# Kernel tuning notes

Hardware: AMD Instinct MI355X
Metric: run time of the kernel (lower is better)

Reference implementation:

```python
import jax, jax.numpy as jnp
import numpy as np

B, T, NE = 8, 4096, 1024
E, TOPK = 16, 2
LIN = NE + 32 + NE // 4 + NE // 4 + NE // 8 + NE // 8  # 1824
N_CITIES = 4


def setup_inputs() -> dict:
    key = jax.random.key(0)
    ks = jax.random.split(key, 11)
    s = 1.0 / np.sqrt(LIN)
    return {
        "mh_output": jax.random.normal(ks[0], (B, T, NE), jnp.float32),
        "delta_t_info": jax.random.normal(ks[1], (B, T, NE // 4), jnp.float32),
        "delta_dis_info": jax.random.normal(ks[2], (B, T, NE // 4), jnp.float32),
        "delta_rg_info": jax.random.normal(ks[3], (B, T, NE // 8), jnp.float32),
        "delta_entropy_info": jax.random.normal(ks[4], (B, T, NE // 8), jnp.float32),
        "city_embeddings": jax.random.normal(ks[5], (N_CITIES, 32), jnp.float32),
        "w_route": jax.random.uniform(ks[6], (LIN, E), jnp.float32, -s, s),
        "b_route": jax.random.uniform(ks[7], (E,), jnp.float32, -s, s),
        "w_noise": jax.random.uniform(ks[8], (LIN, E), jnp.float32, -s, s),
        "b_noise": jax.random.uniform(ks[9], (E,), jnp.float32, -s, s),
        "noise_eps": jax.random.normal(ks[10], (B, T, E), jnp.float32),
        "city_index": 0,
    }


def reference(mh_output, delta_t_info, delta_dis_info, delta_rg_info,
              delta_entropy_info, city_embeddings, w_route, b_route,
              w_noise, b_noise, noise_eps, city_index):
    b, t, _ = mh_output.shape
    city_embed = city_embeddings[city_index]  # [32]
    city_embeds = jnp.broadcast_to(city_embed[None, None, :], (b, t, 32))
    x = jnp.concatenate([mh_output, city_embeds, delta_t_info, delta_dis_info,
                         delta_rg_info, delta_entropy_info], axis=-1)  # [B,T,LIN]
    logits = jnp.einsum('btf,fe->bte', x, w_route) + b_route
    noise_logits = jnp.einsum('btf,fe->bte', x, w_noise) + b_noise
    noisy_logits = logits + noise_eps * jax.nn.softplus(noise_logits)  # training path
    gate1 = jax.nn.softmax(noisy_logits, axis=-1)
    top_k_logits, indices = jax.lax.top_k(noisy_logits, TOPK)  # [B,T,K]
    # scatter top-k values into a -inf tensor == mask non-topk entries to -inf
    mask = jnp.sum(jax.nn.one_hot(indices, noisy_logits.shape[-1], dtype=jnp.bool_), axis=-2) > 0
    sparse_logits = jnp.where(mask, noisy_logits, -jnp.inf)
    router_output = jax.nn.softmax(sparse_logits, axis=-1)
    return router_output, indices, gate1
```

## Files before the change

### kernel.cpp

```cpp
#include <hip/hip_runtime.h>
#include <math.h>


#define TOKS 128
#define NCHUNK 28
#define I_OFF 524288
#define G_OFF 589824
#define SA 68
#define SW 36
#define SS 36

__device__ __forceinline__ float softplus_f(float x) {
  return fmaxf(x, 0.0f) + log1pf(expf(-fabsf(x)));
}

__device__ __forceinline__ float get_comp(const float4& v, int kk) {
  return kk == 0 ? v.x : kk == 1 ? v.y : kk == 2 ? v.z : v.w;
}

__global__ __launch_bounds__(512, 2) void router_kernel(
    const float* __restrict__ mh, const float* __restrict__ dt,
    const float* __restrict__ dd, const float* __restrict__ rg,
    const float* __restrict__ de, const float* __restrict__ cemb_all,
    const float* __restrict__ w_route, const float* __restrict__ b_route,
    const float* __restrict__ w_noise, const float* __restrict__ b_noise,
    const float* __restrict__ eps, const int* __restrict__ city_index,
    float* __restrict__ out) {
  __shared__ float smem[22016];
  __shared__ float city_l[32];
  float* sA0 = smem;
  float* sA1 = smem + 8704;
  float* sW0 = smem + 17408;
  float* sW1 = smem + 19712;
  float* sS  = smem;

  const int tid = threadIdx.x;
  const int w   = tid >> 6;
  const int ln  = tid & 63;
  const int tg  = ln & 15;
  const int eg  = ln >> 4;
  const int blockTok = blockIdx.x * TOKS;

  if (tid < 32) {
    const int e = tid & 15;
    const float* wsrc = (tid < 16) ? w_route : w_noise;
    const float* bsrc = (tid < 16) ? b_route : b_noise;
    const float* ce = cemb_all + city_index[0] * 32;
    float s = bsrc[e];
#pragma unroll
    for (int j = 0; j < 32; ++j) s = fmaf(ce[j], wsrc[(1024 + j) * 16 + e], s);
    city_l[tid] = s;
  }

  float4 accL[8], accH[8];
#pragma unroll
  for (int j = 0; j < 8; ++j) {
    accL[j] = make_float4(0.f, 0.f, 0.f, 0.f);
    accH[j] = make_float4(0.f, 0.f, 0.f, 0.f);
  }

  const int arow = tid >> 4, acol = (tid & 15) * 4;
  const int wrow = tid >> 3, wcol = tid & 7;

  float4 AR0, AR1, AR2, AR3, WR;

  auto a_src = [&](int g, int row) -> const float* {
    const float* base; int stride;
    if (g < 16)      { base = mh + g * 64;        stride = 1024; }
    else if (g < 20) { base = dt + (g - 16) * 64; stride = 256; }
    else if (g < 24) { base = dd + (g - 20) * 64; stride = 256; }
    else if (g < 26) { base = rg + (g - 24) * 64; stride = 128; }
    else             { base = de + (g - 26) * 64; stride = 128; }
    return base + (size_t)(blockTok + row) * stride;
  };

  auto prefetch = [&](int g) {
    AR0 = *(const float4*)(a_src(g, arow +  0) + acol);
    AR1 = *(const float4*)(a_src(g, arow + 32) + acol);
    AR2 = *(const float4*)(a_src(g, arow + 64) + acol);
    AR3 = *(const float4*)(a_src(g, arow + 96) + acol);
    const int kb = g * 64 + ((g >= 16) ? 32 : 0);
    const float* ws = (wcol < 4)
        ? (w_route + (kb + wrow) * 16 + wcol * 4)
        : (w_noise + (kb + wrow) * 16 + (wcol - 4) * 4);
    WR = *(const float4*)ws;
  };

  auto stage = [&](float* A, float* W) {
    *(float4*)&A[(arow +  0) * SA + acol] = AR0;
    *(float4*)&A[(arow + 32) * SA + acol] = AR1;
    *(float4*)&A[(arow + 64) * SA + acol] = AR2;
    *(float4*)&A[(arow + 96) * SA + acol] = AR3;
    *(float4*)&W[wrow * SW + wcol * 4] = WR;
  };

  prefetch(0);
  stage(sA0, sW0);
  __syncthreads();

  for (int c = 0; c < NCHUNK; ++c) {
    const float* A = (c & 1) ? sA1 : sA0;
    const float* W = (c & 1) ? sW1 : sW0;

    if (c + 1 < NCHUNK) prefetch(c + 1);

    const int k0 = w * 8;
#pragma unroll
    for (int q = 0; q < 2; ++q) {
      const int koff = k0 + q * 4;
      float4 a[8];
#pragma unroll
      for (int j = 0; j < 8; ++j)
        a[j] = *(const float4*)&A[(tg + 16 * j) * SA + koff];
#pragma unroll
      for (int kk = 0; kk < 4; ++kk) {
        float4 wv0 = *(const float4*)&W[(koff + kk) * SW + eg * 8];
        float4 wv1 = *(const float4*)&W[(koff + kk) * SW + eg * 8 + 4];
#pragma unroll
        for (int j = 0; j < 8; ++j) {
          const float s = get_comp(a[j], kk);
          accL[j].x = fmaf(s, wv0.x, accL[j].x);
          accL[j].y = fmaf(s, wv0.y, accL[j].y);
          accL[j].z = fmaf(s, wv0.z, accL[j].z);
          accL[j].w = fmaf(s, wv0.w, accL[j].w);
          accH[j].x = fmaf(s, wv1.x, accH[j].x);
          accH[j].y = fmaf(s, wv1.y, accH[j].y);
          accH[j].z = fmaf(s, wv1.z, accH[j].z);
          accH[j].w = fmaf(s, wv1.w, accH[j].w);
        }
      }
    }

    if (c + 1 < NCHUNK) stage((c & 1) ? sA0 : sA1, (c & 1) ? sW0 : sW1);
    __syncthreads();
  }

  for (int r = 0; r < 8; ++r) {
    if (w == r) {
#pragma unroll
      for (int j = 0; j < 8; ++j) {
        float* p = &sS[(tg + 16 * j) * SS + eg * 8];
        if (r == 0) {
          *(float4*)(p)     = accL[j];
          *(float4*)(p + 4) = accH[j];
        } else {
          float4 x0 = *(float4*)(p), x1 = *(float4*)(p + 4);
          x0.x += accL[j].x; x0.y += accL[j].y; x0.z += accL[j].z; x0.w += accL[j].w;
          x1.x += accH[j].x; x1.y += accH[j].y; x1.z += accH[j].z; x1.w += accH[j].w;
          *(float4*)(p)     = x0;
          *(float4*)(p + 4) = x1;
        }
      }
    }
    __syncthreads();
  }

  if (tid < TOKS) {
    const int tokg = blockTok + tid;
    float l[32];
#pragma unroll
    for (int e4 = 0; e4 < 8; ++e4) {
      float4 s0 = *(const float4*)&sS[tid * SS + e4 * 4];
      l[e4 * 4 + 0] = s0.x + ((e4 * 4 + 0 < 32) ? 0.f : 0.f);
      l[e4 * 4 + 0] = s0.x; l[e4 * 4 + 1] = s0.y;
      l[e4 * 4 + 2] = s0.z; l[e4 * 4 + 3] = s0.w;
    }
#pragma unroll
    for (int e = 0; e < 32; ++e) l[e] += city_l[e];

    const float* ep = eps + (size_t)tokg * 16;
    float n[16];
#pragma unroll
    for (int e = 0; e < 16; ++e)
      n[e] = fmaf(ep[e], softplus_f(l[16 + e]), l[e]);

    float m1 = -INFINITY; int i1 = 0;
#pragma unroll
    for (int e = 0; e < 16; ++e)
      if (n[e] > m1) { m1 = n[e]; i1 = e; }
    float m2 = -INFINITY; int i2 = 0;
#pragma unroll
    for (int e = 0; e < 16; ++e)
      if (e != i1 && n[e] > m2) { m2 = n[e]; i2 = e; }

    float ex[16], Z = 0.f;
#pragma unroll
    for (int e = 0; e < 16; ++e) { ex[e] = expf(n[e] - m1); Z += ex[e]; }
    const float invZ  = 1.0f / Z;
    const float invZ2 = 1.0f / (1.0f + expf(m2 - m1));

    float r[16], g1[16];
#pragma unroll
    for (int e = 0; e < 16; ++e) {
      r[e]  = (e == i1 || e == i2) ? ex[e] * invZ2 : 0.0f;
      g1[e] = ex[e] * invZ;
    }

    float* ro = out + (size_t)tokg * 16;
#pragma unroll
    for (int e4 = 0; e4 < 4; ++e4)
      *(float4*)(ro + e4 * 4) = make_float4(r[e4*4], r[e4*4+1], r[e4*4+2], r[e4*4+3]);

    out[I_OFF + (size_t)tokg * 2 + 0] = (float)i1;
    out[I_OFF + (size_t)tokg * 2 + 1] = (float)i2;

    float* go = out + G_OFF + (size_t)tokg * 16;
#pragma unroll
    for (int e4 = 0; e4 < 4; ++e4)
      *(float4*)(go + e4 * 4) = make_float4(g1[e4*4], g1[e4*4+1], g1[e4*4+2], g1[e4*4+3]);
  }
}

extern "C" void kernel_launch(void* const* d_in, const int* in_sizes, int n_in,
                              void* d_out, int out_size, void* d_ws, size_t ws_size,
                              hipStream_t stream) {
  const float* mh = (const float*)d_in[0];
  const float* dt = (const float*)d_in[1];
  const float* dd = (const float*)d_in[2];
  const float* rg = (const float*)d_in[3];
  const float* de = (const float*)d_in[4];
  const float* ce = (const float*)d_in[5];
  const float* wr = (const float*)d_in[6];
  const float* br = (const float*)d_in[7];
  const float* wn = (const float*)d_in[8];
  const float* bn = (const float*)d_in[9];
  const float* ep = (const float*)d_in[10];
  const int*   ci = (const int*)d_in[11];
  float* out = (float*)d_out;

  router_kernel<<<256, 512, 0, stream>>>(mh, dt, dd, rg, de, ce, wr, br, wn, bn,
                                         ep, ci, out);
}
```

Measured before the change: 296.5 us.

## Stage tiles via direct global-to-LDS DMA with swizzle and halve tokens per block

Replaces register-staged global loads with global_load_lds DMA into an XOR-swizzled, unpadded LDS layout. Tokens per block drop from 128 to 64, doubling the grid to 512 blocks and shrinking LDS so two blocks fit per CU. The aim is more memory-level parallelism and occupancy for this bandwidth-bound GEMV-like router. Per-token arithmetic intensity of weight reuse falls, and there is a full vmcnt wait per chunk.

Measured after the change: 295.0 us. Within noise of the previous version (-0.5%).

```diff
diff --git a/kernel.cpp b/kernel.cpp
--- a/kernel.cpp
+++ b/kernel.cpp
@@ -2,12 +2,10 @@
 #include <math.h>
 
 
-#define TOKS 128
+#define TOKS 64
 #define NCHUNK 28
 #define I_OFF 524288
 #define G_OFF 589824
-#define SA 68
-#define SW 36
 #define SS 36
 
 __device__ __forceinline__ float softplus_f(float x) {
@@ -16,6 +14,12 @@
 
 __device__ __forceinline__ float get_comp(const float4& v, int kk) {
   return kk == 0 ? v.x : kk == 1 ? v.y : kk == 2 ? v.z : v.w;
+}
+
+__device__ __forceinline__ void dma16(const float* g, float* l) {
+  __builtin_amdgcn_global_load_lds(
+      (const __attribute__((address_space(1))) void*)g,
+      (__attribute__((address_space(3))) void*)l, 16, 0, 0);
 }
 
 __global__ __launch_bounds__(512, 2) void router_kernel(
@@ -26,13 +30,13 @@
     const float* __restrict__ w_noise, const float* __restrict__ b_noise,
     const float* __restrict__ eps, const int* __restrict__ city_index,
     float* __restrict__ out) {
-  __shared__ float smem[22016];
-  __shared__ float city_l[32];
+  __shared__ float smem[12288];
   float* sA0 = smem;
-  float* sA1 = smem + 8704;
-  float* sW0 = smem + 17408;
-  float* sW1 = smem + 19712;
+  float* sA1 = smem + 4096;
+  float* sW0 = smem + 8192;
+  float* sW1 = smem + 10240;
   float* sS  = smem;
+  float* cityL = smem + 2304;
 
   const int tid = threadIdx.x;
   const int w   = tid >> 6;
@@ -41,83 +45,71 @@
   const int eg  = ln >> 4;
   const int blockTok = blockIdx.x * TOKS;
 
-  if (tid < 32) {
-    const int e = tid & 15;
-    const float* wsrc = (tid < 16) ? w_route : w_noise;
-    const float* bsrc = (tid < 16) ? b_route : b_noise;
-    const float* ce = cemb_all + city_index[0] * 32;
-    float s = bsrc[e];
-#pragma unroll
-    for (int j = 0; j < 32; ++j) s = fmaf(ce[j], wsrc[(1024 + j) * 16 + e], s);
-    city_l[tid] = s;
-  }
-
-  float4 accL[8], accH[8];
-#pragma unroll
-  for (int j = 0; j < 8; ++j) {
+  float4 accL[4], accH[4];
+#pragma unroll
+  for (int j = 0; j < 4; ++j) {
     accL[j] = make_float4(0.f, 0.f, 0.f, 0.f);
     accH[j] = make_float4(0.f, 0.f, 0.f, 0.f);
   }
-
-  const int arow = tid >> 4, acol = (tid & 15) * 4;
-  const int wrow = tid >> 3, wcol = tid & 7;
-
-  float4 AR0, AR1, AR2, AR3, WR;
 
   auto a_src = [&](int g, int row) -> const float* {
     const float* base; int stride;
     if (g < 16)      { base = mh + g * 64;        stride = 1024; }
     else if (g < 20) { base = dt + (g - 16) * 64; stride = 256; }
     else if (g < 24) { base = dd + (g - 20) * 64; stride = 256; }
-    else if (g < 26) { base = rg + (g - 24) * 64; stride = 128; }
-    else             { base = de + (g - 26) * 64; stride = 128; }
+    else             { base = (g < 26) ? rg + (g - 24) * 64
+                                       : de + (g - 26) * 64;
+                       stride = 128; }
     return base + (size_t)(blockTok + row) * stride;
   };
 
-  auto prefetch = [&](int g) {
-    AR0 = *(const float4*)(a_src(g, arow +  0) + acol);
-    AR1 = *(const float4*)(a_src(g, arow + 32) + acol);
-    AR2 = *(const float4*)(a_src(g, arow + 64) + acol);
-    AR3 = *(const float4*)(a_src(g, arow + 96) + acol);
-    const int kb = g * 64 + ((g >= 16) ? 32 : 0);
-    const float* ws = (wcol < 4)
-        ? (w_route + (kb + wrow) * 16 + wcol * 4)
-        : (w_noise + (kb + wrow) * 16 + (wcol - 4) * 4);
-    WR = *(const float4*)ws;
+  auto stageDMA = [&](int g, float* Abuf, float* Wbuf) {
+#pragma unroll
+    for (int i = 0; i < 2; ++i) {
+      const int slot = i * 512 + tid;
+      const int r    = slot >> 4;
+      const int c4   = (slot & 15) ^ (r & 15);
+      dma16(a_src(g, r) + c4 * 4, Abuf + slot * 4);
+    }
+    {
+      const int r  = tid >> 3;
+      const int c4 = tid & 7;
+      const int kb = g * 64 + ((g >= 16) ? 32 : 0) + r;
+      const float* ws = (c4 < 4) ? (w_route + kb * 16 + c4 * 4)
+                                 : (w_noise + kb * 16 + (c4 - 4) * 4);
+      dma16(ws, Wbuf + tid * 4);
+    }
   };
 
-  auto stage = [&](float* A, float* W) {
-    *(float4*)&A[(arow +  0) * SA + acol] = AR0;
-    *(float4*)&A[(arow + 32) * SA + acol] = AR1;
-    *(float4*)&A[(arow + 64) * SA + acol] = AR2;
-    *(float4*)&A[(arow + 96) * SA + acol] = AR3;
-    *(float4*)&W[wrow * SW + wcol * 4] = WR;
-  };
-
-  prefetch(0);
-  stage(sA0, sW0);
+  stageDMA(0, sA0, sW0);
+  asm volatile("s_waitcnt vmcnt(0)" ::: "memory");
   __syncthreads();
+
+  const int c4x0 = (((w << 1) | 0) ^ tg) << 2;
+  const int c4x1 = (((w << 1) | 1) ^ tg) << 2;
+  const int k0 = w * 8;
 
   for (int c = 0; c < NCHUNK; ++c) {
     const float* A = (c & 1) ? sA1 : sA0;
     const float* W = (c & 1) ? sW1 : sW0;
 
-    if (c + 1 < NCHUNK) prefetch(c + 1);
-
-    const int k0 = w * 8;
+    if (c + 1 < NCHUNK)
+      stageDMA(c + 1, (c & 1) ? sA0 : sA1, (c & 1) ? sW0 : sW1);
+
 #pragma unroll
     for (int q = 0; q < 2; ++q) {
-      const int koff = k0 + q * 4;
-      float4 a[8];
-#pragma unroll
-      for (int j = 0; j < 8; ++j)
-        a[j] = *(const float4*)&A[(tg + 16 * j) * SA + koff];
+      const int cofs = q ? c4x1 : c4x0;
+      float4 a[4];
+#pragma unroll
+      for (int j = 0; j < 4; ++j)
+        a[j] = *(const float4*)&A[(tg + 16 * j) * 64 + cofs];
 #pragma unroll
       for (int kk = 0; kk < 4; ++kk) {
-        float4 wv0 = *(const float4*)&W[(koff + kk) * SW + eg * 8];
-        float4 wv1 = *(const float4*)&W[(koff + kk) * SW + eg * 8 + 4];
-#pragma unroll
-        for (int j = 0; j < 8; ++j) {
+        const int krow = k0 + q * 4 + kk;
+        float4 wv0 = *(const float4*)&W[krow * 32 + eg * 8];
+        float4 wv1 = *(const float4*)&W[krow * 32 + eg * 8 + 4];
+#pragma unroll
+        for (int j = 0; j < 4; ++j) {
           const float s = get_comp(a[j], kk);
           accL[j].x = fmaf(s, wv0.x, accL[j].x);
           accL[j].y = fmaf(s, wv0.y, accL[j].y);
@@ -131,14 +123,26 @@
       }
     }
 
-    if (c + 1 < NCHUNK) stage((c & 1) ? sA0 : sA1, (c & 1) ? sW0 : sW1);
+    asm volatile("s_waitcnt vmcnt(0)" ::: "memory");
     __syncthreads();
+  }
+
+  if (tid < 32) {
+    const int e = tid & 15;
+    const float* wsrc = (tid < 16) ? w_route : w_noise;
+    const float* bsrc = (tid < 16) ? b_route : b_noise;
+    const float* ce = cemb_all + city_index[0] * 32;
+    float sacc = bsrc[e];
+#pragma unroll
+    for (int j = 0; j < 32; ++j)
+      sacc = fmaf(ce[j], wsrc[(1024 + j) * 16 + e], sacc);
+    cityL[tid] = sacc;
   }
 
   for (int r = 0; r < 8; ++r) {
     if (w == r) {
 #pragma unroll
-      for (int j = 0; j < 8; ++j) {
+      for (int j = 0; j < 4; ++j) {
         float* p = &sS[(tg + 16 * j) * SS + eg * 8];
         if (r == 0) {
           *(float4*)(p)     = accL[j];
@@ -161,12 +165,11 @@
 #pragma unroll
     for (int e4 = 0; e4 < 8; ++e4) {
       float4 s0 = *(const float4*)&sS[tid * SS + e4 * 4];
-      l[e4 * 4 + 0] = s0.x + ((e4 * 4 + 0 < 32) ? 0.f : 0.f);
       l[e4 * 4 + 0] = s0.x; l[e4 * 4 + 1] = s0.y;
       l[e4 * 4 + 2] = s0.z; l[e4 * 4 + 3] = s0.w;
     }
 #pragma unroll
-    for (int e = 0; e < 32; ++e) l[e] += city_l[e];
+    for (int e = 0; e < 32; ++e) l[e] += cityL[e];
 
     const float* ep = eps + (size_t)tokg * 16;
     float n[16];
@@ -228,6 +231,6 @@
   const int*   ci = (const int*)d_in[11];
   float* out = (float*)d_out;
 
-  router_kernel<<<256, 512, 0, stream>>>(mh, dt, dd, rg, de, ce, wr, br, wn, bn,
+  router_kernel<<<512, 512, 0, stream>>>(mh, dt, dd, rg, de, ce, wr, br, wn, bn,
                                          ep, ci, out);
 }
```
